# Kernel tuning notes

Hardware: AMD Instinct MI355X
Metric: run time of the kernel (lower is better)

## Reference

```python
import jax, jax.numpy as jnp
import numpy as np

N_NODES = 50000
N_EDGES = 800000
IN_CH = 16
HEADS = 4
OUT_CH = 128
NEG_SLOPE = 0.2  # GATv2Conv default negative_slope


def setup_inputs() -> dict:
    key = jax.random.key(0)
    k1, k2, k3, k4, k5, k6 = jax.random.split(key, 6)
    edge_feat = jax.random.normal(k1, (N_NODES, IN_CH), dtype=jnp.float32)
    edge_index = jax.random.randint(k2, (2, N_EDGES), 0, N_NODES, dtype=jnp.int64)
    s = 1.0 / np.sqrt(IN_CH)
    W_l = jax.random.normal(k3, (IN_CH, HEADS * OUT_CH), dtype=jnp.float32) * s
    W_r = jax.random.normal(k4, (IN_CH, HEADS * OUT_CH), dtype=jnp.float32) * s
    att = jax.random.normal(k5, (HEADS, OUT_CH), dtype=jnp.float32) * (1.0 / np.sqrt(OUT_CH))
    bias = jnp.zeros((HEADS * OUT_CH,), dtype=jnp.float32)
    return {"edge_feat": edge_feat, "edge_index": edge_index,
            "W_l": W_l, "W_r": W_r, "att": att, "bias": bias}


def reference(edge_feat, edge_index, W_l, W_r, att, bias):
    # GATv2Conv forward (eval mode: dropout is identity), concat=True,
    # add_self_loops=True (PyG default).
    N = edge_feat.shape[0]
    loops = jnp.arange(N, dtype=edge_index.dtype)
    ei = jnp.concatenate([edge_index, jnp.stack([loops, loops])], axis=1)
    src, dst = ei[0], ei[1]  # message flows src -> dst

    x_l = (edge_feat @ W_l).reshape(N, HEADS, OUT_CH)  # source transform
    x_r = (edge_feat @ W_r).reshape(N, HEADS, OUT_CH)  # target transform

    # edge-wise GATv2 score: a^T LeakyReLU(x_l[j] + x_r[i])
    e = jax.nn.leaky_relu(x_l[src] + x_r[dst], NEG_SLOPE)  # [E, H, C]
    score = jnp.einsum('ehc,hc->eh', e, att)               # [E, H]

    # segment softmax over incoming edges of each target node
    smax = jax.ops.segment_max(score, dst, num_segments=N)  # [N, H]
    ex = jnp.exp(score - smax[dst])
    denom = jax.ops.segment_sum(ex, dst, num_segments=N)    # [N, H]
    alpha = ex / (denom[dst] + 1e-16)                       # [E, H]

    # scatter-aggregate weighted source features
    out = jax.ops.segment_sum(alpha[:, :, None] * x_l[src], dst, num_segments=N)
    return out.reshape(N, HEADS * OUT_CH) + bias
```

## Files before the change

### kernel.cpp

```cpp
#include <hip/hip_runtime.h>
#include <math.h>

#define N_NODES 50000
#define N_EDGES 800000
#define FDIM 512
#define NEG_SLOPE 0.2f
#define CAP 64

#define GEMM_BLKS 782
#define FILL_BLKS 3125

typedef _Float16 v2h __attribute__((ext_vector_type(2)));
typedef _Float16 v8h __attribute__((ext_vector_type(8)));
typedef float f32x4 __attribute__((ext_vector_type(4)));

__device__ __forceinline__ v2h pack_h2(float a, float b) {
    v2h r; r.x = (_Float16)a; r.y = (_Float16)b; return r;
}

__global__ __launch_bounds__(256) void preproc_kernel(const float* __restrict__ feat,
                                                      const float* __restrict__ Wl,
                                                      unsigned int* __restrict__ xlb,
                                                      const int* __restrict__ ei,
                                                      int* __restrict__ deg,
                                                      int* __restrict__ bucket) {
    int t = threadIdx.x;
    if (blockIdx.x >= GEMM_BLKS) {
        bool is64 = true;
#pragma unroll
        for (int i = 0; i < 16; i++) is64 = is64 && (ei[2 * i + 1] == 0);
        int e = (blockIdx.x - GEMM_BLKS) * 256 + t;
        if (e < N_EDGES) {
            int src = is64 ? ei[2 * e] : ei[e];
            int dst = is64 ? ei[2 * (N_EDGES + e)] : ei[N_EDGES + e];
            int pos = atomicAdd(&deg[dst], 1);
            if (pos < CAP) bucket[dst * CAP + pos] = src;
        }
        return;
    }

    __shared__ float fsh[64 * 16];
    int node0 = blockIdx.x * 64;
    int nvalid = min(64, N_NODES - node0);

    float w0[16], w1[16];
#pragma unroll
    for (int k = 0; k < 16; k++) {
        float2 w = ((const float2*)(Wl + k * FDIM))[t];
        w0[k] = w.x; w1[k] = w.y;
    }
    if (t < nvalid * 4) {
        ((float4*)fsh)[t] = ((const float4*)(feat + (size_t)node0 * 16))[t];
    }
    __syncthreads();

    for (int n = 0; n < nvalid; n++) {
        const float4* fq = (const float4*)(fsh + n * 16);
        float4 q0 = fq[0], q1 = fq[1], q2 = fq[2], q3 = fq[3];
        float fr[16] = {q0.x, q0.y, q0.z, q0.w, q1.x, q1.y, q1.z, q1.w,
                        q2.x, q2.y, q2.z, q2.w, q3.x, q3.y, q3.z, q3.w};
        float a0 = 0.f, a1 = 0.f;
#pragma unroll
        for (int k = 0; k < 16; k++) {
            a0 = fmaf(fr[k], w0[k], a0);
            a1 = fmaf(fr[k], w1[k], a1);
        }
        v2h hv = pack_h2(a0, a1);
        xlb[(size_t)(node0 + n) * 256 + t] = __builtin_bit_cast(unsigned int, hv);
    }
}

#define DPP_ROR_ADD(x, ctrl) \
    ((x) + __int_as_float(__builtin_amdgcn_update_dpp(0, __float_as_int(x), (ctrl), 0xF, 0xF, true)))

__device__ __forceinline__ float score8(uint4 u, const v2h* __restrict__ xr2,
                                        const v2h* __restrict__ a2, v2h sl) {
    v2h x0 = __builtin_bit_cast(v2h, u.x);
    v2h x1 = __builtin_bit_cast(v2h, u.y);
    v2h x2 = __builtin_bit_cast(v2h, u.z);
    v2h x3 = __builtin_bit_cast(v2h, u.w);
#if __has_builtin(__builtin_amdgcn_fdot2)
    float ps = 0.f;
    v2h s;
    s = x0 + xr2[0]; s = __builtin_elementwise_max(s, s * sl);
    ps = __builtin_amdgcn_fdot2(s, a2[0], ps, false);
    s = x1 + xr2[1]; s = __builtin_elementwise_max(s, s * sl);
    ps = __builtin_amdgcn_fdot2(s, a2[1], ps, false);
    s = x2 + xr2[2]; s = __builtin_elementwise_max(s, s * sl);
    ps = __builtin_amdgcn_fdot2(s, a2[2], ps, false);
    s = x3 + xr2[3]; s = __builtin_elementwise_max(s, s * sl);
    ps = __builtin_amdgcn_fdot2(s, a2[3], ps, false);
    return ps;
#else
    v2h ps = {(_Float16)0.f, (_Float16)0.f};
    v2h s;
    s = x0 + xr2[0]; ps += __builtin_elementwise_max(s, s * sl) * a2[0];
    s = x1 + xr2[1]; ps += __builtin_elementwise_max(s, s * sl) * a2[1];
    s = x2 + xr2[2]; ps += __builtin_elementwise_max(s, s * sl) * a2[2];
    s = x3 + xr2[3]; ps += __builtin_elementwise_max(s, s * sl) * a2[3];
    return (float)ps.x + (float)ps.y;
#endif
}

__device__ __forceinline__ void load_batch(const int* __restrict__ brow, int k, int dn,
                                           int node, const char* __restrict__ xlb_b,
                                           unsigned lane16, uint4* __restrict__ u) {
    int4 q = *(const int4*)(brow + k);
    unsigned o0 = ((unsigned)((k     < dn) ? q.x : node) << 10) + lane16;
    unsigned o1 = ((unsigned)((k + 1 < dn) ? q.y : node) << 10) + lane16;
    unsigned o2 = ((unsigned)((k + 2 < dn) ? q.z : node) << 10) + lane16;
    unsigned o3 = ((unsigned)((k + 3 < dn) ? q.w : node) << 10) + lane16;
    u[0] = *(const uint4*)(xlb_b + o0);
    u[1] = *(const uint4*)(xlb_b + o1);
    u[2] = *(const uint4*)(xlb_b + o2);
    u[3] = *(const uint4*)(xlb_b + o3);
}

__device__ __forceinline__ void process_batch(const uint4* __restrict__ u, int r,
                                              const v2h* __restrict__ xr2,
                                              const v2h* __restrict__ a2, v2h sl,
                                              float* __restrict__ acc,
                                              float& m, float& d) {
    float p0 = score8(u[0], xr2, a2, sl);
    float p1 = score8(u[1], xr2, a2, sl);
    float p2 = score8(u[2], xr2, a2, sl);
    float p3 = score8(u[3], xr2, a2, sl);

    p0 = DPP_ROR_ADD(p0, 0x128); p1 = DPP_ROR_ADD(p1, 0x128);
    p2 = DPP_ROR_ADD(p2, 0x128); p3 = DPP_ROR_ADD(p3, 0x128);
    p0 = DPP_ROR_ADD(p0, 0x124); p1 = DPP_ROR_ADD(p1, 0x124);
    p2 = DPP_ROR_ADD(p2, 0x124); p3 = DPP_ROR_ADD(p3, 0x124);
    p0 = DPP_ROR_ADD(p0, 0x122); p1 = DPP_ROR_ADD(p1, 0x122);
    p2 = DPP_ROR_ADD(p2, 0x122); p3 = DPP_ROR_ADD(p3, 0x122);
    p0 = DPP_ROR_ADD(p0, 0x121); p1 = DPP_ROR_ADD(p1, 0x121);
    p2 = DPP_ROR_ADD(p2, 0x121); p3 = DPP_ROR_ADD(p3, 0x121);

    if (r < 2) p1 = -INFINITY;
    if (r < 3) p2 = -INFINITY;
    if (r < 4) p3 = -INFINITY;

    float nm = fmaxf(fmaxf(fmaxf(m, p0), fmaxf(p1, p2)), p3);
    float sc = __expf(m - nm);
    float w0 = __expf(p0 - nm);
    float w1 = __expf(p1 - nm);
    float w2 = __expf(p2 - nm);
    float w3 = __expf(p3 - nm);
    d = fmaf(d, sc, (w0 + w1) + (w2 + w3));

    v8h h0 = __builtin_bit_cast(v8h, u[0]);
    v8h h1 = __builtin_bit_cast(v8h, u[1]);
    v8h h2 = __builtin_bit_cast(v8h, u[2]);
    v8h h3 = __builtin_bit_cast(v8h, u[3]);
#pragma unroll
    for (int j = 0; j < 8; j++) {
        float v = acc[j] * sc;
        v = fmaf(w0, (float)h0[j], v);
        v = fmaf(w1, (float)h1[j], v);
        v = fmaf(w2, (float)h2[j], v);
        v = fmaf(w3, (float)h3[j], v);
        acc[j] = v;
    }
    m = nm;
}

__global__ __launch_bounds__(512) void gat_aggregate_kernel(
        const float* __restrict__ feat, const float* __restrict__ Wr,
        const float* __restrict__ att,  const float* __restrict__ bias,
        const char* __restrict__ xlb_b, const int* __restrict__ deg,
        const int* __restrict__ bucket, float* __restrict__ out) {
    int t = threadIdx.x;
    int wave = t >> 6, lane = t & 63;
    int node = blockIdx.x * 8 + wave;
    int cbase = lane * 8;
    unsigned lane16 = (unsigned)lane << 4;

    float f[16];
    {
        const float4* fp = (const float4*)(feat + (size_t)node * 16);
        float4 f0 = fp[0], f1 = fp[1], f2 = fp[2], f3 = fp[3];
        f[0]=f0.x; f[1]=f0.y; f[2]=f0.z; f[3]=f0.w;
        f[4]=f1.x; f[5]=f1.y; f[6]=f1.z; f[7]=f1.w;
        f[8]=f2.x; f[9]=f2.y; f[10]=f2.z; f[11]=f2.w;
        f[12]=f3.x; f[13]=f3.y; f[14]=f3.z; f[15]=f3.w;
    }

    float xr[8];
#pragma unroll
    for (int j = 0; j < 8; j++) xr[j] = 0.f;
#pragma unroll
    for (int k = 0; k < 16; k++) {
        float fk = f[k];
        float4 wa = *(const float4*)(Wr + k * FDIM + cbase);
        float4 wb = *(const float4*)(Wr + k * FDIM + cbase + 4);
        xr[0] = fmaf(fk, wa.x, xr[0]); xr[1] = fmaf(fk, wa.y, xr[1]);
        xr[2] = fmaf(fk, wa.z, xr[2]); xr[3] = fmaf(fk, wa.w, xr[3]);
        xr[4] = fmaf(fk, wb.x, xr[4]); xr[5] = fmaf(fk, wb.y, xr[5]);
        xr[6] = fmaf(fk, wb.z, xr[6]); xr[7] = fmaf(fk, wb.w, xr[7]);
    }
    v2h xr2[4];
    xr2[0] = pack_h2(xr[0], xr[1]);
    xr2[1] = pack_h2(xr[2], xr[3]);
    xr2[2] = pack_h2(xr[4], xr[5]);
    xr2[3] = pack_h2(xr[6], xr[7]);

    v2h a2[4];
    {
        float4 a0 = *(const float4*)(att + cbase);
        float4 a1 = *(const float4*)(att + cbase + 4);
        a2[0] = pack_h2(a0.x, a0.y);
        a2[1] = pack_h2(a0.z, a0.w);
        a2[2] = pack_h2(a1.x, a1.y);
        a2[3] = pack_h2(a1.z, a1.w);
    }
    const v2h sl = {(_Float16)NEG_SLOPE, (_Float16)NEG_SLOPE};

    float m = -INFINITY, d = 0.f;
    float acc[8];
#pragma unroll
    for (int j = 0; j < 8; j++) acc[j] = 0.f;

    int dn = min(deg[node], CAP);
    int total = dn + 1;
    const int* brow = bucket + node * CAP;

    uint4 A[4], B[4];
    load_batch(brow, 0, dn, node, xlb_b, lane16, A);
    int k = 0;
    while (true) {
        int kB = k + 4;
        bool hasB = kB < total;
        if (hasB) load_batch(brow, kB, dn, node, xlb_b, lane16, B);
        process_batch(A, total - k, xr2, a2, sl, acc, m, d);
        if (!hasB) break;
        int kA = k + 8;
        bool hasA = kA < total;
        if (hasA) load_batch(brow, kA, dn, node, xlb_b, lane16, A);
        process_batch(B, total - kB, xr2, a2, sl, acc, m, d);
        if (!hasA) break;
        k = kA;
    }

    float inv = 1.f / (d + 1e-16f);
    float4 b0 = *(const float4*)(bias + cbase);
    float4 b1 = *(const float4*)(bias + cbase + 4);
    float bb[8] = {b0.x, b0.y, b0.z, b0.w, b1.x, b1.y, b1.z, b1.w};
    float o[8];
#pragma unroll
    for (int j = 0; j < 8; j++) o[j] = fmaf(acc[j], inv, bb[j]);
    float* op = out + (size_t)node * FDIM + cbase;
    f32x4 ov0 = {o[0], o[1], o[2], o[3]};
    f32x4 ov1 = {o[4], o[5], o[6], o[7]};
    __builtin_nontemporal_store(ov0, (f32x4*)op);
    __builtin_nontemporal_store(ov1, (f32x4*)(op + 4));
}

extern "C" void kernel_launch(void* const* d_in, const int* in_sizes, int n_in,
                              void* d_out, int out_size, void* d_ws, size_t ws_size,
                              hipStream_t stream) {
    const float* feat = (const float*)d_in[0];
    const int*   ei   = (const int*)d_in[1];
    const float* Wl   = (const float*)d_in[2];
    const float* Wr   = (const float*)d_in[3];
    const float* att  = (const float*)d_in[4];
    const float* bias = (const float*)d_in[5];
    float* out = (float*)d_out;

    char* ws = (char*)d_ws;
    size_t off = 0;
    unsigned int* xlb = (unsigned int*)(ws + off); off += (size_t)N_NODES * 256 * sizeof(unsigned int);
    int* deg    = (int*)(ws + off); off += (size_t)N_NODES * sizeof(int);
    int* bucket = (int*)(ws + off); off += ((size_t)N_NODES * CAP + 16) * sizeof(int);
    (void)ws_size; (void)in_sizes; (void)n_in; (void)out_size;

    hipError_t _e = hipMemsetAsync(deg, 0, (size_t)N_NODES * sizeof(int), stream); (void)_e;
    preproc_kernel<<<GEMM_BLKS + FILL_BLKS, 256, 0, stream>>>(feat, Wl, xlb, ei, deg, bucket);
    gat_aggregate_kernel<<<N_NODES / 8, 512, 0, stream>>>(
        feat, Wr, att, bias, (const char*)xlb, deg, bucket, out);
}
```

Measured before the change: 322.8 us.

## Pad degree counters, use exp2 with prescaled attention, raise occupancy bound

Spreads each node's degree counter onto its own 64-byte slot so concurrent atomics on neighbouring nodes no longer contend on the same cache line. Folds log2(e) into the attention vector so the softmax can call the hardware exp2 instruction directly. Adds a min-blocks hint to the aggregate kernel's launch bounds to push toward higher occupancy. The padding makes the memset 16x larger and spreads the degree reads, and the occupancy hint may force register spills.

Result: slower. 552.9 us (+71.3%).

```diff
diff --git a/kernel.cpp b/kernel.cpp
--- a/kernel.cpp
+++ b/kernel.cpp
@@ -9,10 +9,18 @@
 
 #define GEMM_BLKS 782
 #define FILL_BLKS 3125
+#define DEG_PAD_SHIFT 4
 
 typedef _Float16 v2h __attribute__((ext_vector_type(2)));
 typedef _Float16 v8h __attribute__((ext_vector_type(8)));
 typedef float f32x4 __attribute__((ext_vector_type(4)));
+
+#if __has_builtin(__builtin_amdgcn_exp2f)
+#define EXP2(x) __builtin_amdgcn_exp2f(x)
+#else
+#define EXP2(x) __expf((x) * 0.69314718056f)
+#endif
+#define LOG2E 1.44269504089f
 
 __device__ __forceinline__ v2h pack_h2(float a, float b) {
     v2h r; r.x = (_Float16)a; r.y = (_Float16)b; return r;
@@ -33,7 +41,7 @@
         if (e < N_EDGES) {
             int src = is64 ? ei[2 * e] : ei[e];
             int dst = is64 ? ei[2 * (N_EDGES + e)] : ei[N_EDGES + e];
-            int pos = atomicAdd(&deg[dst], 1);
+            int pos = atomicAdd(&deg[dst << DEG_PAD_SHIFT], 1);
             if (pos < CAP) bucket[dst * CAP + pos] = src;
         }
         return;
@@ -140,11 +148,11 @@
     if (r < 4) p3 = -INFINITY;
 
     float nm = fmaxf(fmaxf(fmaxf(m, p0), fmaxf(p1, p2)), p3);
-    float sc = __expf(m - nm);
-    float w0 = __expf(p0 - nm);
-    float w1 = __expf(p1 - nm);
-    float w2 = __expf(p2 - nm);
-    float w3 = __expf(p3 - nm);
+    float sc = EXP2(m - nm);
+    float w0 = EXP2(p0 - nm);
+    float w1 = EXP2(p1 - nm);
+    float w2 = EXP2(p2 - nm);
+    float w3 = EXP2(p3 - nm);
     d = fmaf(d, sc, (w0 + w1) + (w2 + w3));
 
     v8h h0 = __builtin_bit_cast(v8h, u[0]);
@@ -163,7 +171,7 @@
     m = nm;
 }
 
-__global__ __launch_bounds__(512) void gat_aggregate_kernel(
+__global__ __launch_bounds__(512, 8) void gat_aggregate_kernel(
         const float* __restrict__ feat, const float* __restrict__ Wr,
         const float* __restrict__ att,  const float* __restrict__ bias,
         const char* __restrict__ xlb_b, const int* __restrict__ deg,
@@ -207,10 +215,10 @@
     {
         float4 a0 = *(const float4*)(att + cbase);
         float4 a1 = *(const float4*)(att + cbase + 4);
-        a2[0] = pack_h2(a0.x, a0.y);
-        a2[1] = pack_h2(a0.z, a0.w);
-        a2[2] = pack_h2(a1.x, a1.y);
-        a2[3] = pack_h2(a1.z, a1.w);
+        a2[0] = pack_h2(a0.x * LOG2E, a0.y * LOG2E);
+        a2[1] = pack_h2(a0.z * LOG2E, a0.w * LOG2E);
+        a2[2] = pack_h2(a1.x * LOG2E, a1.y * LOG2E);
+        a2[3] = pack_h2(a1.z * LOG2E, a1.w * LOG2E);
     }
     const v2h sl = {(_Float16)NEG_SLOPE, (_Float16)NEG_SLOPE};
 
@@ -219,7 +227,7 @@
 #pragma unroll
     for (int j = 0; j < 8; j++) acc[j] = 0.f;
 
-    int dn = min(deg[node], CAP);
+    int dn = min(deg[node << DEG_PAD_SHIFT], CAP);
     int total = dn + 1;
     const int* brow = bucket + node * CAP;
 
@@ -268,11 +276,11 @@
     char* ws = (char*)d_ws;
     size_t off = 0;
     unsigned int* xlb = (unsigned int*)(ws + off); off += (size_t)N_NODES * 256 * sizeof(unsigned int);
-    int* deg    = (int*)(ws + off); off += (size_t)N_NODES * sizeof(int);
+    int* deg    = (int*)(ws + off); off += ((size_t)N_NODES << DEG_PAD_SHIFT) * sizeof(int);
     int* bucket = (int*)(ws + off); off += ((size_t)N_NODES * CAP + 16) * sizeof(int);
     (void)ws_size; (void)in_sizes; (void)n_in; (void)out_size;
 
-    hipError_t _e = hipMemsetAsync(deg, 0, (size_t)N_NODES * sizeof(int), stream); (void)_e;
+    hipError_t _e = hipMemsetAsync(deg, 0, ((size_t)N_NODES << DEG_PAD_SHIFT) * sizeof(int), stream); (void)_e;
     preproc_kernel<<<GEMM_BLKS + FILL_BLKS, 256, 0, stream>>>(feat, Wl, xlb, ei, deg, bucket);
     gat_aggregate_kernel<<<N_NODES / 8, 512, 0, stream>>>(
         feat, Wr, att, bias, (const char*)xlb, deg, bucket, out);
```
